# Performance work log

Measured on AMD Instinct MI355X. Metric: run time of the kernel, lower is better.

The kernel has to match this reference:

```python
import jax, jax.numpy as jnp
import numpy as np

GROUP_NORM_EPSILON = 1e-06
NUM_GROUPS = 32


def group_norm(x, gamma, beta, num_groups, eps):
    # x: [B, H, W, C]; normalize over (H, W, C//G) within each group.
    B, H, W, C = x.shape
    xg = x.reshape(B, H, W, num_groups, C // num_groups)
    mean = jnp.mean(xg, axis=(1, 2, 4), keepdims=True)
    var = jnp.mean(jnp.square(xg - mean), axis=(1, 2, 4), keepdims=True)
    xn = (xg - mean) * jax.lax.rsqrt(var + eps)
    return xn.reshape(B, H, W, C) * gamma + beta


def setup_inputs() -> dict:
    key = jax.random.key(0)
    ks = jax.random.split(key, 6)
    B, H, W, C = 4, 64, 64, 512
    scale = 1.0 / np.sqrt(C)
    return {
        "inputs": jax.random.normal(ks[0], (B, H, W, C), dtype=jnp.float32),
        "gamma": jnp.ones((C,), dtype=jnp.float32),
        "beta": jnp.zeros((C,), dtype=jnp.float32),
        "Wq": jax.random.normal(ks[1], (C, C), dtype=jnp.float32) * scale,
        "bq": jnp.zeros((C,), dtype=jnp.float32),
        "Wk": jax.random.normal(ks[2], (C, C), dtype=jnp.float32) * scale,
        "bk": jnp.zeros((C,), dtype=jnp.float32),
        "Wv": jax.random.normal(ks[3], (C, C), dtype=jnp.float32) * scale,
        "bv": jnp.zeros((C,), dtype=jnp.float32),
        "Wo": jax.random.normal(ks[4], (C, C), dtype=jnp.float32) * scale,
        "bo": jnp.zeros((C,), dtype=jnp.float32),
    }


def reference(inputs, gamma, beta, Wq, bq, Wk, bk, Wv, bv, Wo, bo):
    B, H, W, C = inputs.shape
    N = H * W
    h = group_norm(inputs, gamma, beta, NUM_GROUPS, GROUP_NORM_EPSILON)
    hf = h.reshape(B, N, C)  # flatten spatial: [B, N, C]
    q = hf @ Wq + bq
    k = hf @ Wk + bk
    v = hf @ Wv + bv
    # full spatial self-attention: [B, N, N]
    scores = jnp.einsum("bnc,bmc->bnm", q, k) * (C ** -0.5)
    attn = jax.nn.softmax(scores, axis=-1)
    out = jnp.einsum("bnm,bmc->bnc", attn, v)
    out = out @ Wo + bo
    return out.reshape(B, H, W, C) + inputs
```

## Files before the change

### kernel.cpp

```cpp
#include <hip/hip_runtime.h>
#include <hip/hip_bf16.h>

using bf16 = __hip_bfloat16;
using u16  = unsigned short;
typedef __attribute__((ext_vector_type(8))) short s16x8;
typedef __attribute__((ext_vector_type(4))) float f32x4;

__device__ __forceinline__ float b2f(u16 u){
  union{unsigned u; float f;} c; c.u = ((unsigned)u)<<16; return c.f;
}
__device__ __forceinline__ u16 f2b(float f){
  __hip_bfloat16 h = __float2bfloat16(f);
  return *reinterpret_cast<u16*>(&h);
}

#define GLDS16(g, l_) __builtin_amdgcn_global_load_lds( \
    (const __attribute__((address_space(1))) unsigned int*)(g), \
    (__attribute__((address_space(3))) unsigned int*)(l_), 16, 0, 0)

__global__ __launch_bounds__(512) void gn_kernel(const float* __restrict__ x,
    const float* __restrict__ gamma, const float* __restrict__ beta,
    bf16* __restrict__ h)
{
  const int b = blockIdx.x >> 5, g = blockIdx.x & 31;
  const int t = threadIdx.x;
  const size_t base = (size_t)b*4096*512 + (size_t)g*16;
  float sum = 0.f, sq = 0.f;
  for (int i = 0; i < 8; i++){
    const float* p = x + base + (size_t)(i*512 + t)*512;
    #pragma unroll
    for (int j = 0; j < 4; j++){
      f32x4 v = *(const f32x4*)(p + j*4);
      #pragma unroll
      for (int e = 0; e < 4; e++){ sum += v[e]; sq += v[e]*v[e]; }
    }
  }
  __shared__ float red[16];
  for (int o = 32; o > 0; o >>= 1){ sum += __shfl_xor(sum, o); sq += __shfl_xor(sq, o); }
  const int w = t >> 6, l = t & 63;
  if (l == 0){ red[w] = sum; red[8 + w] = sq; }
  __syncthreads();
  if (t == 0){
    float a = 0.f, bb = 0.f;
    for (int i = 0; i < 8; i++){ a += red[i]; bb += red[8 + i]; }
    red[0] = a; red[8] = bb;
  }
  __syncthreads();
  const float inv_n = 1.f/65536.f;
  const float mean = red[0]*inv_n;
  const float var  = red[8]*inv_n - mean*mean;
  const float rstd = rsqrtf(var + 1e-6f);
  float ga[16], be[16];
  #pragma unroll
  for (int j = 0; j < 16; j++){
    ga[j] = gamma[g*16 + j];
    be[j] = beta [g*16 + j];
  }
  u16* hp = (u16*)h;
  for (int i = 0; i < 8; i++){
    const float* p = x + base + (size_t)(i*512 + t)*512;
    u16* q = hp + base + (size_t)(i*512 + t)*512;
    s16x8 o0, o1;
    #pragma unroll
    for (int j = 0; j < 4; j++){
      f32x4 v = *(const f32x4*)(p + j*4);
      #pragma unroll
      for (int e = 0; e < 4; e++){
        int c = j*4 + e;
        u16 r = f2b((v[e] - mean)*rstd*ga[c] + be[c]);
        if (c < 8) o0[c] = (short)r; else o1[c - 8] = (short)r;
      }
    }
    *(s16x8*)q = o0; *(s16x8*)(q + 8) = o1;
  }
}

struct W4 { const float* p[4]; };
__global__ __launch_bounds__(256) void transpose_w4(W4 srcs, bf16* __restrict__ dst)
{
  __shared__ float tile[64][65];
  const float* in = srcs.p[blockIdx.z];
  u16* out = (u16*)dst + (size_t)blockIdx.z*512*512;
  const int tr = blockIdx.y*64, tc = blockIdx.x*64;
  const int t = threadIdx.x;
  #pragma unroll
  for (int i = 0; i < 16; i++){
    int idx = i*256 + t, r = idx >> 6, c = idx & 63;
    tile[r][c] = in[(size_t)(tr + r)*512 + tc + c];
  }
  __syncthreads();
  #pragma unroll
  for (int i = 0; i < 16; i++){
    int idx = i*256 + t, r = idx >> 6, c = idx & 63;
    out[(size_t)(tc + r)*512 + tr + c] = f2b(tile[c][r]);
  }
}

__global__ __launch_bounds__(256) void transpose_v(const u16* __restrict__ qkv,
    bf16* __restrict__ vT)
{
  __shared__ u16 tile[64][72];
  const u16* in = qkv + 1024 + (size_t)blockIdx.z*4096*1536;
  u16* out = (u16*)vT + (size_t)blockIdx.z*512*4096;
  const int tr = blockIdx.y*64, tc = blockIdx.x*64;
  const int t = threadIdx.x;
  #pragma unroll
  for (int i = 0; i < 16; i++){
    int idx = i*256 + t, r = idx >> 6, c = idx & 63;
    tile[r][c] = in[(size_t)(tr + r)*1536 + tc + c];
  }
  __syncthreads();
  #pragma unroll
  for (int i = 0; i < 16; i++){
    int idx = i*256 + t, r = idx >> 6, c = idx & 63;
    out[(size_t)(tc + r)*4096 + tr + c] = tile[c][r];
  }
}

template<int EPI, typename OutT>
__global__ __launch_bounds__(256) void gemm_bt(
    const u16* __restrict__ A, int lda, long sA,
    const u16* __restrict__ Bt, int ldb, long sB,
    OutT* __restrict__ Cmat, int ldc, long sC,
    int K, float scale,
    const float* __restrict__ b0, const float* __restrict__ b1,
    const float* __restrict__ b2, const float* __restrict__ res)
{
  __shared__ u16 As[128*64];
  __shared__ u16 Bs[128*64];
  const int t = threadIdx.x, l = t & 63, w = t >> 6;
  const int wr = w >> 1, wc = w & 1;
  int bx = blockIdx.x, by = blockIdx.y;
  {
    const int gx = gridDim.x, nb = gx * gridDim.y;
    if ((nb & 7) == 0){
      int lin = by*gx + bx;
      int s = (lin & 7)*(nb >> 3) + (lin >> 3);
      bx = s % gx; by = s / gx;
    }
  }
  const int m0 = by * 128, n0 = bx * 128;
  const u16* Au  = A  + (size_t)blockIdx.z * sA;
  const u16* Btu = Bt + (size_t)blockIdx.z * sB;

  f32x4 acc[4][4];
  #pragma unroll
  for (int m = 0; m < 4; m++)
    #pragma unroll
    for (int n = 0; n < 4; n++) acc[m][n] = (f32x4){0.f,0.f,0.f,0.f};

  const int srow = l >> 3;
  const int scol = ((l & 7) ^ srow) * 8;
  const int xorv = (l & 7) << 4;
  const int nkt = K >> 6;
  for (int kt = 0; kt < nkt; ++kt){
    const int k0 = kt << 6;
    #pragma unroll
    for (int j = 0; j < 4; j++){
      const int chunk = w*4 + j;
      const int row = chunk*8 + srow;
      GLDS16(Au  + (size_t)(m0 + row)*lda + k0 + scol, &As[chunk*512]);
      GLDS16(Btu + (size_t)(n0 + row)*ldb + k0 + scol, &Bs[chunk*512]);
    }
    __syncthreads();
    #pragma unroll
    for (int kk = 0; kk < 2; kk++){
      const int kbyte = (kk*64 + (l >> 4)*16) ^ xorv;
      s16x8 af[4], bff[4];
      #pragma unroll
      for (int m = 0; m < 4; m++)
        af[m]  = *(const s16x8*)((const char*)As + (wr*64 + m*16 + (l & 15))*128 + kbyte);
      #pragma unroll
      for (int n = 0; n < 4; n++)
        bff[n] = *(const s16x8*)((const char*)Bs + (wc*64 + n*16 + (l & 15))*128 + kbyte);
      #pragma unroll
      for (int m = 0; m < 4; m++)
        #pragma unroll
        for (int n = 0; n < 4; n++)
          acc[m][n] = __builtin_amdgcn_mfma_f32_16x16x32_bf16(af[m], bff[n], acc[m][n], 0, 0, 0);
    }
    __syncthreads();
  }
  const int lc = l & 15, lr4 = (l >> 4)*4;
  OutT* Cz = Cmat + (size_t)blockIdx.z * sC;
  #pragma unroll
  for (int n = 0; n < 4; n++){
    const int col = n0 + wc*64 + n*16 + lc;
    float bv = 0.f;
    if (EPI & 8){
      const float* bp = (col < 512) ? b0 : (col < 1024 ? b1 : b2);
      bv = bp[col & 511];
    } else if (EPI & 1){
      bv = b0[col];
    }
    #pragma unroll
    for (int m = 0; m < 4; m++){
      const int rowb = m0 + wr*64 + m*16 + lr4;
      #pragma unroll
      for (int r = 0; r < 4; r++){
        float v = acc[m][n][r];
        if (EPI & 2) v *= scale;
        v += bv;
        const size_t off = (size_t)(rowb + r)*ldc + col;
        if (EPI & 4) v += res[off];
        if constexpr (__is_same(OutT, float)) Cz[off] = v;
        else ((u16*)Cz)[off] = f2b(v);
      }
    }
  }
}

template<int EPI, typename OutT>
__global__ __launch_bounds__(512, 2) void gemm256(
    const u16* __restrict__ A, int lda, long sA,
    const u16* __restrict__ Bt, int ldb, long sB,
    OutT* __restrict__ Cmat, int ldc, long sC,
    int K, float scale,
    const float* __restrict__ b0, const float* __restrict__ b1,
    const float* __restrict__ b2, const float* __restrict__ res)
{
  __shared__ u16 L[2][2][2][256*32];
  const int t = threadIdx.x, l = t & 63, w = t >> 3 >> 3;
  const int wm = w >> 2, wn = w & 3;
  int bx = blockIdx.x, by = blockIdx.y;
  {
    const int gx = gridDim.x, nb = gx * gridDim.y;
    if ((nb & 7) == 0){
      int lin = by*gx + bx;
      int s = (lin & 7)*(nb >> 3) + (lin >> 3);
      bx = s % gx; by = s / gx;
    }
  }
  const int m0 = by * 256, n0 = bx * 256;
  const u16* Au  = A  + (size_t)blockIdx.z * sA;
  const u16* Btu = Bt + (size_t)blockIdx.z * sB;

  f32x4 acc[8][4];
  #pragma unroll
  for (int m = 0; m < 8; m++)
    #pragma unroll
    for (int n = 0; n < 4; n++) acc[m][n] = (f32x4){0.f,0.f,0.f,0.f};

  const int srow_s = t >> 2;
  const int sce    = (((t & 3)*16) ^ (((srow_s >> 1) & 3) << 4)) >> 1;
  const int l15 = l & 15, kb16 = (l >> 4)*16;

  int arow[8], brow[4];
  #pragma unroll
  for (int i = 0; i < 8; i++){
    const int r = wm*128 + i*16 + l15;
    arow[i] = r*64 + (kb16 ^ (((r >> 1) & 3) << 4));
  }
  #pragma unroll
  for (int i = 0; i < 4; i++){
    const int r = wn*64 + i*16 + l15;
    brow[i] = r*64 + (kb16 ^ (((r >> 1) & 3) << 4));
  }

#define STG256(HALF, XU, LD, ROW0, COLBASE) do { \
    GLDS16((XU) + (size_t)((ROW0) + srow_s)*(LD) + (COLBASE) + sce, \
           (char*)(HALF) + w*1024); \
    GLDS16((XU) + (size_t)((ROW0) + 128 + srow_s)*(LD) + (COLBASE) + sce, \
           (char*)(HALF) + 8192 + w*1024); \
  } while(0)

#define VMW4 asm volatile("s_waitcnt vmcnt(4)" ::: "memory")

#define PH256(BUF, KK, MQ, STAGE_STMT, WAIT_STMT) do { \
    s16x8 af_[4], bg_[4]; \
    _Pragma("unroll") \
    for (int mf = 0; mf < 4; mf++) \
      af_[mf] = *(const s16x8*)((const char*)&L[BUF][0][KK][0] + arow[(MQ)*4 + mf]); \
    _Pragma("unroll") \
    for (int nf = 0; nf < 4; nf++) \
      bg_[nf] = *(const s16x8*)((const char*)&L[BUF][1][KK][0] + brow[nf]); \
    STAGE_STMT; \
    WAIT_STMT; \
    __builtin_amdgcn_s_barrier(); \
    __builtin_amdgcn_s_setprio(1); \
    _Pragma("unroll") \
    for (int mf = 0; mf < 4; mf++) \
      _Pragma("unroll") \
      for (int nf = 0; nf < 4; nf++) \
        acc[(MQ)*4 + mf][nf] = __builtin_amdgcn_mfma_f32_16x16x32_bf16( \
            af_[mf], bg_[nf], acc[(MQ)*4 + mf][nf], 0, 0, 0); \
    __builtin_amdgcn_s_setprio(0); \
    __builtin_amdgcn_s_barrier(); \
  } while(0)

  const int nkt = K >> 6;
  STG256(&L[0][0][0][0], Au,  lda, m0, 0);
  STG256(&L[0][1][0][0], Btu, ldb, n0, 0);
  STG256(&L[0][0][1][0], Au,  lda, m0, 32);
  STG256(&L[0][1][1][0], Btu, ldb, n0, 32);
  STG256(&L[1][0][0][0], Au,  lda, m0, 64);
  STG256(&L[1][1][0][0], Btu, ldb, n0, 64);
  VMW4;
  __builtin_amdgcn_s_barrier();

  const int niter = nkt >> 1;
  for (int it = 0; it < niter; ++it){
    const int kt1 = 2*it + 1;
    const int kA  = (kt1 + 1 < nkt) ? kt1 + 1 : nkt - 1;
    const int kB  = (kt1 + 2 < nkt) ? kt1 + 2 : nkt - 1;
    PH256(0, 0, 0, STG256(&L[1][0][1][0], Au,  lda, m0, kt1*64 + 32), (void)0);
    PH256(0, 0, 1, STG256(&L[1][1][1][0], Btu, ldb, n0, kt1*64 + 32), (void)0);
    PH256(0, 1, 0, STG256(&L[0][0][0][0], Au,  lda, m0, kA*64),       (void)0);
    PH256(0, 1, 1, STG256(&L[0][1][0][0], Btu, ldb, n0, kA*64),       VMW4);
    PH256(1, 0, 0, STG256(&L[0][0][1][0], Au,  lda, m0, kA*64 + 32),  (void)0);
    PH256(1, 0, 1, STG256(&L[0][1][1][0], Btu, ldb, n0, kA*64 + 32),  (void)0);
    PH256(1, 1, 0, STG256(&L[1][0][0][0], Au,  lda, m0, kB*64),       (void)0);
    PH256(1, 1, 1, STG256(&L[1][1][0][0], Btu, ldb, n0, kB*64),       VMW4);
  }

  const int lc = l15, lr4 = (l >> 4)*4;
  OutT* Cz = Cmat + (size_t)blockIdx.z * sC;
  #pragma unroll
  for (int nf = 0; nf < 4; nf++){
    const int col = n0 + wn*64 + nf*16 + lc;
    float bv = 0.f;
    if (EPI & 8){
      const float* bp = (col < 512) ? b0 : (col < 1024 ? b1 : b2);
      bv = bp[col & 511];
    } else if (EPI & 1){
      bv = b0[col];
    }
    #pragma unroll
    for (int mf = 0; mf < 8; mf++){
      const int rowb = m0 + wm*128 + mf*16 + lr4;
      #pragma unroll
      for (int r = 0; r < 4; r++){
        float v = acc[mf][nf][r];
        if (EPI & 2) v *= scale;
        v += bv;
        const size_t off = (size_t)(rowb + r)*ldc + col;
        if (EPI & 4) v += res[off];
        if constexpr (__is_same(OutT, float)) Cz[off] = v;
        else ((u16*)Cz)[off] = f2b(v);
      }
    }
  }
#undef STG256
#undef VMW4
#undef PH256
}

__global__ __launch_bounds__(512) void pv_fused(
    const u16* __restrict__ S, const u16* __restrict__ vT,
    bf16* __restrict__ ao, int batched, int batch0)
{
  __shared__ u16 Bs[256*64];
  __shared__ u16 Ps[64*64];
  __shared__ float lsArr[64];
  const int t = threadIdx.x, l = t & 63, w = t >> 6;
  int batch, mt, half;
  if (batched){
    const int lin = blockIdx.x, x = lin & 7, s = lin >> 3;
    batch = x >> 1; mt = (s >> 1)*2 + (x & 1); half = s & 1;
  } else { batch = batch0; mt = blockIdx.x >> 1; half = blockIdx.x & 1; }
  const int m0 = mt*64, c0 = half*256;
  const u16* Sb  = S  + (size_t)batch*4096*4096;
  const u16* vTb = vT + (size_t)batch*512*4096 + (size_t)c0*4096;
  u16* aob = (u16*)ao + (size_t)batch*4096*512;

  f32x4 acc[4][2];
  #pragma unroll
  for (int m = 0; m < 4; m++)
    #pragma unroll
    for (int n = 0; n < 2; n++) acc[m][n] = (f32x4){0.f,0.f,0.f,0.f};

  const int srow = l >> 3, lane8 = l & 7;
  const int scol = (lane8 ^ srow) * 8;
  const int xorv = lane8 << 4;
  const int r_loc = w*8 + srow;
  const int smaddr = r_loc*128 + ((lane8*16) ^ (srow << 4));
  float lsumrow = 0.f;

  const u16* Srow = Sb + (size_t)(m0 + r_loc)*4096 + lane8*8;

  #pragma unroll
  for (int j = 0; j < 4; j++){
    const int chunk = w*4 + j;
    const int row = chunk*8 + srow;
    GLDS16(vTb + (size_t)row*4096 + scol, &Bs[chunk*512]);
  }
  s16x8 S_cur = *(const s16x8*)Srow;

  for (int kt = 0; kt < 64; ++kt){
    const int ktn = (kt < 63) ? kt + 1 : 63;
    s16x8 S_next = *(const s16x8*)(Srow + ktn*64);

    float rs = 0.f;
    s16x8 pb;
    #pragma unroll
    for (int j = 0; j < 8; j++){
      const float pvv = exp2f(fminf(b2f((u16)S_cur[j]), 100.f));
      rs += pvv;
      pb[j] = (short)f2b(pvv);
    }
    rs += __shfl_xor(rs, 1); rs += __shfl_xor(rs, 2); rs += __shfl_xor(rs, 4);
    lsumrow += rs;

    *(s16x8*)((char*)Ps + smaddr) = pb;

    asm volatile("s_waitcnt lgkmcnt(0)" ::: "memory");
    __builtin_amdgcn_sched_barrier(0);
    asm volatile("s_waitcnt vmcnt(1)" ::: "memory");
    __builtin_amdgcn_sched_barrier(0);
    __builtin_amdgcn_s_barrier();

    #pragma unroll
    for (int kk = 0; kk < 2; kk++){
      const int kbyte = (kk*64 + (l >> 4)*16) ^ xorv;
      s16x8 pa[4], bf2[2];
      #pragma unroll
      for (int m = 0; m < 4; m++)
        pa[m] = *(const s16x8*)((const char*)Ps + (m*16 + (l & 15))*128 + kbyte);
      #pragma unroll
      for (int n = 0; n < 2; n++)
        bf2[n] = *(const s16x8*)((const char*)Bs + (w*32 + n*16 + (l & 15))*128 + kbyte);
      #pragma unroll
      for (int m = 0; m < 4; m++)
        #pragma unroll
        for (int n = 0; n < 2; n++)
          acc[m][n] = __builtin_amdgcn_mfma_f32_16x16x32_bf16(pa[m], bf2[n], acc[m][n], 0, 0, 0);
    }

    __builtin_amdgcn_sched_barrier(0);
    __builtin_amdgcn_s_barrier();
    __builtin_amdgcn_sched_barrier(0);

    #pragma unroll
    for (int j = 0; j < 4; j++){
      const int chunk = w*4 + j;
      const int row = chunk*8 + srow;
      GLDS16(vTb + (size_t)row*4096 + ktn*64 + scol, &Bs[chunk*512]);
    }
    S_cur = S_next;
  }

  if (lane8 == 0) lsArr[r_loc] = lsumrow;
  __syncthreads();
  #pragma unroll
  for (int m = 0; m < 4; m++){
    const f32x4 lq = *(const f32x4*)&lsArr[m*16 + (l >> 4)*4];
    #pragma unroll
    for (int r = 0; r < 4; r++){
      const float inv = 1.f / lq[r];
      const int row = m0 + m*16 + (l >> 4)*4 + r;
      #pragma unroll
      for (int n = 0; n < 2; n++){
        const int col = c0 + w*32 + n*16 + (l & 15);
        aob[(size_t)row*512 + col] = f2b(acc[m][n][r] * inv);
      }
    }
  }
}

extern "C" void kernel_launch(void* const* d_in, const int* in_sizes, int n_in,
                              void* d_out, int out_size, void* d_ws, size_t ws_size,
                              hipStream_t stream)
{
  (void)in_sizes; (void)n_in; (void)out_size;
  const float* x     = (const float*)d_in[0];
  const float* gamma = (const float*)d_in[1];
  const float* beta  = (const float*)d_in[2];
  const float* Wq = (const float*)d_in[3]; const float* bq = (const float*)d_in[4];
  const float* Wk = (const float*)d_in[5]; const float* bk = (const float*)d_in[6];
  const float* Wv = (const float*)d_in[7]; const float* bv = (const float*)d_in[8];
  const float* Wo = (const float*)d_in[9]; const float* bo = (const float*)d_in[10];
  float* out = (float*)d_out;

  const int B = 4, N = 4096, C = 512;
  const long NC = (long)N*C;
  const float scl2 = 0.04419417382415922f * 1.4426950408889634f;

  char* p0 = (char*)d_ws;
  auto align = [](size_t b){ return (b + 255) & ~(size_t)255; };
  const size_t sz_h   = align((size_t)B*NC*2);
  const size_t sz_w   = align((size_t)4*C*C*2);
  const size_t sz_qkvF= align((size_t)B*N*1536*2);
  const size_t sz_vTF = align((size_t)B*NC*2);
  const size_t sz_aoF = align((size_t)B*NC*2);
  const size_t sz_SF  = align((size_t)B*N*N*2);
  const size_t need_full = sz_h + sz_w + sz_qkvF + sz_vTF + sz_aoF + sz_SF;

  bf16* h    = (bf16*)p0;
  bf16* wAll = (bf16*)(p0 + sz_h);
  char* pv   = p0 + sz_h + sz_w;

  gn_kernel<<<dim3(B*32), dim3(512), 0, stream>>>(x, gamma, beta, h);
  W4 ws4; ws4.p[0] = Wq; ws4.p[1] = Wk; ws4.p[2] = Wv; ws4.p[3] = Wo;
  transpose_w4<<<dim3(8, 8, 4), 256, 0, stream>>>(ws4, wAll);
  bf16* woT = wAll + (size_t)3*C*C;

  if (ws_size >= need_full){
    bf16* qkv = (bf16*)pv;
    bf16* vT  = (bf16*)(pv + sz_qkvF);
    bf16* ao  = (bf16*)(pv + sz_qkvF + sz_vTF);
    bf16* S   = (bf16*)(pv + sz_qkvF + sz_vTF + sz_aoF);

    gemm256<8, bf16><<<dim3(6, 64, 1), 512, 0, stream>>>(
        (const u16*)h, C, 0, (const u16*)wAll, C, 0, qkv, 1536, 0,
        C, 1.f, bq, bk, bv, nullptr);
    transpose_v<<<dim3(8, 64, B), 256, 0, stream>>>((const u16*)qkv, vT);
    gemm256<2, bf16><<<dim3(16, 16, B), 512, 0, stream>>>(
        (const u16*)qkv, 1536, (long)N*1536, (const u16*)qkv + 512, 1536, (long)N*1536,
        S, N, (long)N*N, C, scl2, nullptr, nullptr, nullptr, nullptr);
    pv_fused<<<dim3(512), 512, 0, stream>>>(
        (const u16*)S, (const u16*)vT, ao, 1, 0);
    gemm_bt<5, float><<<dim3(4, 128, 1), 256, 0, stream>>>(
        (const u16*)ao, C, 0, (const u16*)woT, C, 0, out, C, 0,
        C, 1.f, bo, nullptr, nullptr, x);
  } else {
    const size_t sz_qkv1 = align((size_t)N*1536*2);
    const size_t sz_vT1  = align((size_t)NC*2);
    const size_t sz_ao1  = align((size_t)NC*2);
    bf16* qkv = (bf16*)pv;
    bf16* vT  = (bf16*)(pv + sz_qkv1);
    bf16* ao  = (bf16*)(pv + sz_qkv1 + sz_vT1);
    bf16* S   = (bf16*)(pv + sz_qkv1 + sz_vT1 + sz_ao1);
    for (int b = 0; b < B; b++){
      const u16* hb = (const u16*)h + (size_t)b*NC;
      gemm256<8, bf16><<<dim3(6, 16, 1), 512, 0, stream>>>(
          hb, C, 0, (const u16*)wAll, C, 0, qkv, 1536, 0,
          C, 1.f, bq, bk, bv, nullptr);
      transpose_v<<<dim3(8, 64, 1), 256, 0, stream>>>((const u16*)qkv, vT);
      gemm256<2, bf16><<<dim3(16, 16, 1), 512, 0, stream>>>(
          (const u16*)qkv, 1536, 0, (const u16*)qkv + 512, 1536, 0,
          S, N, 0, C, scl2, nullptr, nullptr, nullptr, nullptr);
      pv_fused<<<dim3(128), 512, 0, stream>>>(
          (const u16*)S, (const u16*)vT, ao, 0, b);
      gemm_bt<5, float><<<dim3(4, 32, 1), 256, 0, stream>>>(
          (const u16*)ao, C, 0, (const u16*)woT, C, 0, out + (size_t)b*NC, C, 0,
          C, 1.f, bo, nullptr, nullptr, x + (size_t)b*NC);
    }
  }
}
```

Before: 424.6 us.

## Fuse V transpose into QKV GEMM epilogue with LDS-staged vectorized stores

The QKV projection GEMM now stages its output tile in LDS with an XOR swizzle and writes Q and K as separate contiguous arrays. V is written already transposed, so the standalone transpose_v kernel and its extra read and write of V are removed. The GEMM epilogues now issue 16-byte vector stores instead of scattered 2-byte stores. The P·V kernel also defers its cross-lane row-sum shuffles to after the loop. The costs are an extra LDS round trip and barrier in the epilogue, and strided gather reads from LDS for the transposed V path.

```diff
diff --git a/kernel.cpp b/kernel.cpp
--- a/kernel.cpp
+++ b/kernel.cpp
@@ -96,35 +96,13 @@
   }
 }
 
-__global__ __launch_bounds__(256) void transpose_v(const u16* __restrict__ qkv,
-    bf16* __restrict__ vT)
-{
-  __shared__ u16 tile[64][72];
-  const u16* in = qkv + 1024 + (size_t)blockIdx.z*4096*1536;
-  u16* out = (u16*)vT + (size_t)blockIdx.z*512*4096;
-  const int tr = blockIdx.y*64, tc = blockIdx.x*64;
-  const int t = threadIdx.x;
-  #pragma unroll
-  for (int i = 0; i < 16; i++){
-    int idx = i*256 + t, r = idx >> 6, c = idx & 63;
-    tile[r][c] = in[(size_t)(tr + r)*1536 + tc + c];
-  }
-  __syncthreads();
-  #pragma unroll
-  for (int i = 0; i < 16; i++){
-    int idx = i*256 + t, r = idx >> 6, c = idx & 63;
-    out[(size_t)(tc + r)*4096 + tr + c] = tile[c][r];
-  }
-}
-
 template<int EPI, typename OutT>
 __global__ __launch_bounds__(256) void gemm_bt(
     const u16* __restrict__ A, int lda, long sA,
     const u16* __restrict__ Bt, int ldb, long sB,
     OutT* __restrict__ Cmat, int ldc, long sC,
     int K, float scale,
-    const float* __restrict__ b0, const float* __restrict__ b1,
-    const float* __restrict__ b2, const float* __restrict__ res)
+    const float* __restrict__ b0, const float* __restrict__ res)
 {
   __shared__ u16 As[128*64];
   __shared__ u16 Bs[128*64];
@@ -186,13 +164,7 @@
   #pragma unroll
   for (int n = 0; n < 4; n++){
     const int col = n0 + wc*64 + n*16 + lc;
-    float bv = 0.f;
-    if (EPI & 8){
-      const float* bp = (col < 512) ? b0 : (col < 1024 ? b1 : b2);
-      bv = bp[col & 511];
-    } else if (EPI & 1){
-      bv = b0[col];
-    }
+    const float bv = (EPI & 1) ? b0[col] : 0.f;
     #pragma unroll
     for (int m = 0; m < 4; m++){
       const int rowb = m0 + wr*64 + m*16 + lr4;
@@ -210,17 +182,18 @@
   }
 }
 
-template<int EPI, typename OutT>
+template<int EPI, int OMODE>
 __global__ __launch_bounds__(512, 2) void gemm256(
     const u16* __restrict__ A, int lda, long sA,
     const u16* __restrict__ Bt, int ldb, long sB,
-    OutT* __restrict__ Cmat, int ldc, long sC,
+    u16* __restrict__ C0, int ldc, long sC,
+    u16* __restrict__ C1, u16* __restrict__ C2,
     int K, float scale,
     const float* __restrict__ b0, const float* __restrict__ b1,
-    const float* __restrict__ b2, const float* __restrict__ res)
+    const float* __restrict__ b2)
 {
   __shared__ u16 L[2][2][2][256*32];
-  const int t = threadIdx.x, l = t & 63, w = t >> 3 >> 3;
+  const int t = threadIdx.x, l = t & 63, w = t >> 6;
   const int wm = w >> 2, wn = w & 3;
   int bx = blockIdx.x, by = blockIdx.y;
   {
@@ -313,30 +286,71 @@
     PH256(1, 1, 1, STG256(&L[1][1][0][0], Btu, ldb, n0, kB*64),       VMW4);
   }
 
-  const int lc = l15, lr4 = (l >> 4)*4;
-  OutT* Cz = Cmat + (size_t)blockIdx.z * sC;
+  asm volatile("s_waitcnt vmcnt(0)" ::: "memory");
+  __builtin_amdgcn_s_barrier();
+  u16* Lb = (u16*)&L[0][0][0][0];
+  const int lr4 = (l >> 4)*4;
   #pragma unroll
   for (int nf = 0; nf < 4; nf++){
-    const int col = n0 + wn*64 + nf*16 + lc;
+    const int cloc = wn*64 + nf*16 + l15;
+    const int colg = n0 + cloc;
     float bv = 0.f;
     if (EPI & 8){
-      const float* bp = (col < 512) ? b0 : (col < 1024 ? b1 : b2);
-      bv = bp[col & 511];
-    } else if (EPI & 1){
-      bv = b0[col];
-    }
+      const float* bp = (colg < 512) ? b0 : (colg < 1024 ? b1 : b2);
+      bv = bp[colg & 511];
+    } else if (EPI & 1) bv = b0[colg];
     #pragma unroll
     for (int mf = 0; mf < 8; mf++){
-      const int rowb = m0 + wm*128 + mf*16 + lr4;
+      const int rl0 = wm*128 + mf*16 + lr4;
       #pragma unroll
       for (int r = 0; r < 4; r++){
         float v = acc[mf][nf][r];
         if (EPI & 2) v *= scale;
         v += bv;
-        const size_t off = (size_t)(rowb + r)*ldc + col;
-        if (EPI & 4) v += res[off];
-        if constexpr (__is_same(OutT, float)) Cz[off] = v;
-        else ((u16*)Cz)[off] = f2b(v);
+        const int row = rl0 + r;
+        const int byte = row*512 + ((cloc*2) ^ (((row >> 3) & 7) << 4));
+        *(u16*)((char*)Lb + byte) = f2b(v);
+      }
+    }
+  }
+  __syncthreads();
+  if (OMODE == 0){
+    u16* Cz = C0 + (size_t)blockIdx.z * sC;
+    #pragma unroll
+    for (int i = 0; i < 16; i++){
+      const int idx = i*512 + t;
+      const int row = idx >> 5, cb = (idx & 31)*16;
+      const int byte = row*512 + (cb ^ (((row >> 3) & 7) << 4));
+      s16x8 v = *(const s16x8*)((const char*)Lb + byte);
+      *(s16x8*)(Cz + (size_t)(m0 + row)*ldc + n0 + (cb >> 1)) = v;
+    }
+  } else {
+    const int sec = n0 >> 9, wc0 = n0 & 511;
+    if (sec < 2){
+      u16* dst = (sec == 0) ? C0 : C1;
+      #pragma unroll
+      for (int i = 0; i < 16; i++){
+        const int idx = i*512 + t;
+        const int row = idx >> 5, cb = (idx & 31)*16;
+        const int byte = row*512 + (cb ^ (((row >> 3) & 7) << 4));
+        s16x8 v = *(const s16x8*)((const char*)Lb + byte);
+        *(s16x8*)(dst + (size_t)(m0 + row)*512 + wc0 + (cb >> 1)) = v;
+      }
+    } else {
+      const int batch = m0 >> 12, ntok = m0 & 4095;
+      u16* dst = C2 + (size_t)batch*512*4096;
+      #pragma unroll
+      for (int i = 0; i < 16; i++){
+        const int idx = i*512 + t;
+        const int c_loc = idx >> 5, rseg = (idx & 31)*8;
+        s16x8 v;
+        #pragma unroll
+        for (int j = 0; j < 8; j++){
+          const int row = rseg + j;
+          const int byte = row*512 + ((c_loc*2) ^ (((row >> 3) & 7) << 4));
+          v[j] = *(const short*)((const char*)Lb + byte);
+        }
+        *(s16x8*)(dst + (size_t)(wc0 + c_loc)*4096 + ntok + rseg) = v;
       }
     }
   }
@@ -390,16 +404,13 @@
     const int ktn = (kt < 63) ? kt + 1 : 63;
     s16x8 S_next = *(const s16x8*)(Srow + ktn*64);
 
-    float rs = 0.f;
     s16x8 pb;
     #pragma unroll
     for (int j = 0; j < 8; j++){
       const float pvv = exp2f(fminf(b2f((u16)S_cur[j]), 100.f));
-      rs += pvv;
+      lsumrow += pvv;
       pb[j] = (short)f2b(pvv);
     }
-    rs += __shfl_xor(rs, 1); rs += __shfl_xor(rs, 2); rs += __shfl_xor(rs, 4);
-    lsumrow += rs;
 
     *(s16x8*)((char*)Ps + smaddr) = pb;
 
@@ -439,6 +450,9 @@
     S_cur = S_next;
   }
 
+  lsumrow += __shfl_xor(lsumrow, 1);
+  lsumrow += __shfl_xor(lsumrow, 2);
+  lsumrow += __shfl_xor(lsumrow, 4);
   if (lane8 == 0) lsArr[r_loc] = lsumrow;
   __syncthreads();
   #pragma unroll
@@ -477,63 +491,58 @@
 
   char* p0 = (char*)d_ws;
   auto align = [](size_t b){ return (b + 255) & ~(size_t)255; };
-  const size_t sz_h   = align((size_t)B*NC*2);
-  const size_t sz_w   = align((size_t)4*C*C*2);
-  const size_t sz_qkvF= align((size_t)B*N*1536*2);
-  const size_t sz_vTF = align((size_t)B*NC*2);
-  const size_t sz_aoF = align((size_t)B*NC*2);
-  const size_t sz_SF  = align((size_t)B*N*N*2);
-  const size_t need_full = sz_h + sz_w + sz_qkvF + sz_vTF + sz_aoF + sz_SF;
+  const size_t sz_h  = align((size_t)B*NC*2);
+  const size_t sz_w  = align((size_t)4*C*C*2);
+  const size_t sz_q  = align((size_t)B*NC*2);
+  const size_t sz_S  = align((size_t)B*N*N*2);
+  const size_t need_full = sz_h + sz_w + 4*sz_q + sz_S;
 
   bf16* h    = (bf16*)p0;
   bf16* wAll = (bf16*)(p0 + sz_h);
   char* pv   = p0 + sz_h + sz_w;
+  bf16* woT  = wAll + (size_t)3*C*C;
 
   gn_kernel<<<dim3(B*32), dim3(512), 0, stream>>>(x, gamma, beta, h);
   W4 ws4; ws4.p[0] = Wq; ws4.p[1] = Wk; ws4.p[2] = Wv; ws4.p[3] = Wo;
   transpose_w4<<<dim3(8, 8, 4), 256, 0, stream>>>(ws4, wAll);
-  bf16* woT = wAll + (size_t)3*C*C;
 
   if (ws_size >= need_full){
-    bf16* qkv = (bf16*)pv;
-    bf16* vT  = (bf16*)(pv + sz_qkvF);
-    bf16* ao  = (bf16*)(pv + sz_qkvF + sz_vTF);
-    bf16* S   = (bf16*)(pv + sz_qkvF + sz_vTF + sz_aoF);
-
-    gemm256<8, bf16><<<dim3(6, 64, 1), 512, 0, stream>>>(
-        (const u16*)h, C, 0, (const u16*)wAll, C, 0, qkv, 1536, 0,
-        C, 1.f, bq, bk, bv, nullptr);
-    transpose_v<<<dim3(8, 64, B), 256, 0, stream>>>((const u16*)qkv, vT);
-    gemm256<2, bf16><<<dim3(16, 16, B), 512, 0, stream>>>(
-        (const u16*)qkv, 1536, (long)N*1536, (const u16*)qkv + 512, 1536, (long)N*1536,
-        S, N, (long)N*N, C, scl2, nullptr, nullptr, nullptr, nullptr);
+    u16* q  = (u16*)pv;
+    u16* k  = (u16*)(pv + sz_q);
+    u16* vT = (u16*)(pv + 2*sz_q);
+    u16* ao = (u16*)(pv + 3*sz_q);
+    u16* S  = (u16*)(pv + 4*sz_q);
+
+    gemm256<8, 1><<<dim3(6, 64, 1), 512, 0, stream>>>(
+        (const u16*)h, C, 0, (const u16*)wAll, C, 0,
+        q, 0, 0, k, vT, C, 1.f, bq, bk, bv);
+    gemm256<2, 0><<<dim3(16, 16, B), 512, 0, stream>>>(
+        q, C, NC, k, C, NC, S, N, (long)N*N, nullptr, nullptr,
+        C, scl2, nullptr, nullptr, nullptr);
     pv_fused<<<dim3(512), 512, 0, stream>>>(
-        (const u16*)S, (const u16*)vT, ao, 1, 0);
+        S, vT, (bf16*)ao, 1, 0);
     gemm_bt<5, float><<<dim3(4, 128, 1), 256, 0, stream>>>(
-        (const u16*)ao, C, 0, (const u16*)woT, C, 0, out, C, 0,
-        C, 1.f, bo, nullptr, nullptr, x);
+        ao, C, 0, (const u16*)woT, C, 0, out, C, 0,
+        C, 1.f, bo, x);
   } else {
-    const size_t sz_qkv1 = align((size_t)N*1536*2);
-    const size_t sz_vT1  = align((size_t)NC*2);
-    const size_t sz_ao1  = align((size_t)NC*2);
-    bf16* qkv = (bf16*)pv;
-    bf16* vT  = (bf16*)(pv + sz_qkv1);
-    bf16* ao  = (bf16*)(pv + sz_qkv1 + sz_vT1);
-    bf16* S   = (bf16*)(pv + sz_qkv1 + sz_vT1 + sz_ao1);
+    u16* q  = (u16*)pv;
+    u16* k  = (u16*)(pv + sz_q/4 + 256);
+    u16* vT = (u16*)(pv + 2*(sz_q/4 + 256));
+    u16* ao = (u16*)(pv + 3*(sz_q/4 + 256));
+    u16* S  = (u16*)(pv + 4*(sz_q/4 + 256));
     for (int b = 0; b < B; b++){
       const u16* hb = (const u16*)h + (size_t)b*NC;
-      gemm256<8, bf16><<<dim3(6, 16, 1), 512, 0, stream>>>(
-          hb, C, 0, (const u16*)wAll, C, 0, qkv, 1536, 0,
-          C, 1.f, bq, bk, bv, nullptr);
-      transpose_v<<<dim3(8, 64, 1), 256, 0, stream>>>((const u16*)qkv, vT);
-      gemm256<2, bf16><<<dim3(16, 16, 1), 512, 0, stream>>>(
-          (const u16*)qkv, 1536, 0, (const u16*)qkv + 512, 1536, 0,
-          S, N, 0, C, scl2, nullptr, nullptr, nullptr, nullptr);
+      gemm256<8, 1><<<dim3(6, 16, 1), 512, 0, stream>>>(
+          hb, C, 0, (const u16*)wAll, C, 0,
+          q, 0, 0, k, vT, C, 1.f, bq, bk, bv);
+      gemm256<2, 0><<<dim3(16, 16, 1), 512, 0, stream>>>(
+          q, C, 0, k, C, 0, S, N, 0, nullptr, nullptr,
+          C, scl2, nullptr, nullptr, nullptr);
       pv_fused<<<dim3(128), 512, 0, stream>>>(
-          (const u16*)S, (const u16*)vT, ao, 0, b);
+          S, vT, (bf16*)ao, 0, 0);
       gemm_bt<5, float><<<dim3(4, 32, 1), 256, 0, stream>>>(
-          (const u16*)ao, C, 0, (const u16*)woT, C, 0, out + (size_t)b*NC, C, 0,
-          C, 1.f, bo, nullptr, nullptr, x + (size_t)b*NC);
-    }
-  }
-}
+          ao, C, 0, (const u16*)woT, C, 0, out + (size_t)b*NC, C, 0,
+          C, 1.f, bo, x + (size_t)b*NC);
+    }
+  }
+}
```

Measured after the change: 401.6 us. 1.06x faster.
